# Optimization experiments

Hardware: AMD Instinct MI355X
Metric: run time of the kernel (lower is better)

Reference implementation:

```python
import jax, jax.numpy as jnp
import numpy as np

B, S, D = 2, 2048, 1024
H, DH = 16, 64  # num_heads, attention_dim


def setup_inputs() -> dict:
    key = jax.random.key(0)
    ks = jax.random.split(key, 10)
    x = jax.random.normal(ks[0], (B, S, D), dtype=jnp.float32)
    # causal mask, broadcast over batch and heads (mask==0 -> -inf)
    mask = jnp.tril(jnp.ones((S, S), dtype=jnp.int32))[None, None]
    s = 1.0 / np.sqrt(D)
    Wq = jax.random.normal(ks[1], (D, H * DH), dtype=jnp.float32) * s
    bq = jnp.zeros((H * DH,), dtype=jnp.float32)
    Wk = jax.random.normal(ks[2], (D, H * DH), dtype=jnp.float32) * s
    bk = jnp.zeros((H * DH,), dtype=jnp.float32)
    Wv = jax.random.normal(ks[3], (D, H * DH), dtype=jnp.float32) * s
    bv = jnp.zeros((H * DH,), dtype=jnp.float32)
    Wo = jax.random.normal(ks[4], (H * DH, D), dtype=jnp.float32) * (1.0 / np.sqrt(H * DH))
    bo = jnp.zeros((D,), dtype=jnp.float32)
    return {"x": x, "mask": mask, "Wq": Wq, "bq": bq, "Wk": Wk, "bk": bk,
            "Wv": Wv, "bv": bv, "Wo": Wo, "bo": bo}


def reference(x, mask, Wq, bq, Wk, bk, Wv, bv, Wo, bo):
    b, s, _ = x.shape
    q = (x @ Wq + bq).reshape(b, s, H, DH)
    k = (x @ Wk + bk).reshape(b, s, H, DH)
    v = (x @ Wv + bv).reshape(b, s, H, DH)
    # scores: [B, H, S, S]
    scores = jnp.einsum("bshd,bthd->bhst", q, k) / jnp.sqrt(jnp.float32(DH))
    scores = jnp.where(mask == 0, -jnp.inf, scores)
    w = jax.nn.softmax(scores, axis=-1)
    attended = jnp.einsum("bhst,bthd->bshd", w, v).reshape(b, s, H * DH)
    return attended @ Wo + bo
```

## Files before the change

### kernel.cpp

```cpp
#include <hip/hip_runtime.h>
#include <hip/hip_bf16.h>

#define B_ 2
#define S_ 2048
#define D_ 1024
#define H_ 16
#define DH_ 64

typedef __attribute__((ext_vector_type(8))) short bf16x8;
typedef __attribute__((ext_vector_type(4))) float f32x4;

#define QSCALE 0.18033688011112042f

__device__ __forceinline__ ushort f2b(float f){
  __hip_bfloat16 h = __float2bfloat16(f);
  return *reinterpret_cast<ushort*>(&h);
}

__device__ __forceinline__ unsigned cvtpk(float lo, float hi){
  unsigned r;
  asm("v_cvt_pk_bf16_f32 %0, %1, %2" : "=v"(r) : "v"(lo), "v"(hi));
  return r;
}

__device__ __forceinline__ void gload16(const ushort* g, ushort* l){
  __builtin_amdgcn_global_load_lds((const __attribute__((address_space(1))) unsigned*)g,
                                   (__attribute__((address_space(3))) unsigned*)l, 16, 0, 0);
}

__global__ __launch_bounds__(256) void k_prep(const float* __restrict__ x, ushort* __restrict__ xb,
                                              const float* __restrict__ Wq, const float* __restrict__ Wk,
                                              const float* __restrict__ Wv, const float* __restrict__ Wo,
                                              ushort* __restrict__ WqkvT, ushort* __restrict__ WoT){
  int bid = blockIdx.x, tid = threadIdx.x;
  if (bid < 2048){
    int i = (bid*256 + tid)*8;
    float4 v0 = *(const float4*)(x + i);
    float4 v1 = *(const float4*)(x + i + 4);
    uint4 o;
    o.x = f2b(v0.x) | ((unsigned)f2b(v0.y)<<16);
    o.y = f2b(v0.z) | ((unsigned)f2b(v0.w)<<16);
    o.z = f2b(v1.x) | ((unsigned)f2b(v1.y)<<16);
    o.w = f2b(v1.z) | ((unsigned)f2b(v1.w)<<16);
    *(uint4*)(xb + i) = o;
    return;
  }
  bid -= 2048;
  const int w = bid >> 10, tb = bid & 1023;
  const float* src = (w==0)?Wq:(w==1)?Wk:(w==2)?Wv:Wo;
  ushort* dst = (w==3)?WoT : WqkvT + (size_t)w*(1024*1024);
  __shared__ float tile[32][33];
  const int bx2 = tb & 31, by2 = tb >> 5;
  const int c0 = bx2*32, r0 = by2*32;
  const int tx = tid & 31, ty = tid >> 5;
  #pragma unroll
  for (int i=0;i<4;i++)
    tile[ty + i*8][tx] = src[(size_t)(r0 + ty + i*8)*1024 + c0 + tx];
  __syncthreads();
  #pragma unroll
  for (int i=0;i<4;i++)
    dst[(size_t)(c0 + ty + i*8)*1024 + r0 + tx] = f2b(tile[tx][ty + i*8]);
}

__global__ __launch_bounds__(512, 4) void k_gemm_qkv(const ushort* __restrict__ A,
                                                     const ushort* __restrict__ BT,
                                                     const float* __restrict__ b0p,
                                                     const float* __restrict__ b1p,
                                                     const float* __restrict__ b2p,
                                                     ushort* __restrict__ Cp,
                                                     int M, int N, int K){
  __shared__ ushort As[256*64];
  __shared__ ushort Bs[128*64];
  const int tid = threadIdx.x;
  const int nbn = N >> 7;
  const int bm = blockIdx.x / nbn, bn = blockIdx.x % nbn;
  const int m0 = bm << 8, n0 = bn << 7;
  const int wave = tid >> 6, lane = tid & 63;
  const int wm = (wave >> 1) << 6, wn = (wave & 1) << 6;
  const int lr = lane & 15, lq = lane >> 4;

  f32x4 acc[4][4] = {};

  const int r0 = tid >> 3;
  const int gk = (tid & 7) ^ (r0 & 7);
  const ushort* Agb = A  + (size_t)(m0 + r0)*K + gk*8;
  const ushort* Bgb = BT + (size_t)(n0 + r0)*K + gk*8;
  const int lofs = tid*8;

  for (int kt = 0; kt < K; kt += 64){
    __syncthreads();
    #pragma unroll
    for (int j=0;j<4;j++)
      gload16(Agb + (size_t)j*64*K + kt, &As[lofs + j*4096]);
    #pragma unroll
    for (int j=0;j<2;j++)
      gload16(Bgb + (size_t)j*64*K + kt, &Bs[lofs + j*4096]);
    __syncthreads();
    #pragma unroll
    for (int kk=0;kk<2;kk++){
      bf16x8 af[4], bfr[4];
      #pragma unroll
      for (int i=0;i<4;i++){
        int ra = wm + i*16 + lr;
        af[i]  = *(bf16x8*)&As[ra*64 + (((kk*4+lq) ^ (ra & 7)) << 3)];
        int rb = wn + i*16 + lr;
        bfr[i] = *(bf16x8*)&Bs[rb*64 + (((kk*4+lq) ^ (rb & 7)) << 3)];
      }
      __builtin_amdgcn_s_setprio(1);
      #pragma unroll
      for (int mi=0;mi<4;mi++)
        #pragma unroll
        for (int ni=0;ni<4;ni++)
          acc[mi][ni] = __builtin_amdgcn_mfma_f32_16x16x32_bf16(af[mi], bfr[ni], acc[mi][ni], 0, 0, 0);
      __builtin_amdgcn_s_setprio(0);
    }
  }

  const int seg = n0 >> 10;
  const float* bp = (seg==0 ? b0p : (seg==1 ? b1p : b2p));
  #pragma unroll
  for (int mi=0;mi<4;mi++){
    #pragma unroll
    for (int ni=0;ni<4;ni++){
      int col = n0 + wn + ni*16 + lr;
      int cl = col & 1023;
      float bv = bp[cl];
      int row0 = m0 + wm + mi*16 + lq*4;
      ushort* Qb = Cp;
      if (seg == 0){
        #pragma unroll
        for (int r=0;r<4;r++)
          Qb[(size_t)(row0+r)*1024 + cl] = f2b((acc[mi][ni][r] + bv) * QSCALE);
      } else if (seg == 1){
        ushort* Kb = Qb + (4u<<20);
        #pragma unroll
        for (int r=0;r<4;r++)
          Kb[(size_t)(row0+r)*1024 + cl] = f2b(acc[mi][ni][r] + bv);
      } else {
        ushort* Vt = Qb + (8u<<20);
        int bb = row0 >> 11, srow = row0 & 2047;
        uint2 pk;
        pk.x = cvtpk(acc[mi][ni][0]+bv, acc[mi][ni][1]+bv);
        pk.y = cvtpk(acc[mi][ni][2]+bv, acc[mi][ni][3]+bv);
        *(uint2*)&Vt[((size_t)(bb*1024 + cl))*2048 + srow] = pk;
      }
    }
  }
}

__global__ __launch_bounds__(256) void k_gemm_out(const ushort* __restrict__ A,
                                                  const ushort* __restrict__ BT,
                                                  const float* __restrict__ bias,
                                                  float* __restrict__ Cp,
                                                  int M, int N, int K){
  __shared__ ushort As[128*64];
  __shared__ ushort Bs[128*64];
  const int tid = threadIdx.x;
  const int nbn = N >> 7;
  const int bm = blockIdx.x / nbn, bn = blockIdx.x % nbn;
  const int m0 = bm << 7, n0 = bn << 7;
  const int wave = tid >> 6, lane = tid & 63;
  const int wm = (wave >> 1) << 6, wn = (wave & 1) << 6;
  const int lr = lane & 15, lq = lane >> 4;

  f32x4 acc[4][4] = {};

  const ushort* Ag[4]; const ushort* Bg[4]; int lofs[4];
  #pragma unroll
  for (int j=0;j<4;j++){
    int c = tid + j*256, row = c >> 3, slot = c & 7;
    int gk = slot ^ (row & 7);
    Ag[j] = A  + (size_t)(m0 + row)*K + gk*8;
    Bg[j] = BT + (size_t)(n0 + row)*K + gk*8;
    lofs[j] = c*8;
  }

  for (int kt = 0; kt < K; kt += 64){
    __syncthreads();
    #pragma unroll
    for (int j=0;j<4;j++){
      gload16(Ag[j] + kt, &As[lofs[j]]);
      gload16(Bg[j] + kt, &Bs[lofs[j]]);
    }
    __syncthreads();
    #pragma unroll
    for (int kk=0;kk<2;kk++){
      bf16x8 af[4], bfr[4];
      #pragma unroll
      for (int i=0;i<4;i++){
        int ra = wm + i*16 + lr;
        af[i]  = *(bf16x8*)&As[ra*64 + (((kk*4+lq) ^ (ra & 7)) << 3)];
        int rb = wn + i*16 + lr;
        bfr[i] = *(bf16x8*)&Bs[rb*64 + (((kk*4+lq) ^ (rb & 7)) << 3)];
      }
      __builtin_amdgcn_s_setprio(1);
      #pragma unroll
      for (int mi=0;mi<4;mi++)
        #pragma unroll
        for (int ni=0;ni<4;ni++)
          acc[mi][ni] = __builtin_amdgcn_mfma_f32_16x16x32_bf16(af[mi], bfr[ni], acc[mi][ni], 0, 0, 0);
      __builtin_amdgcn_s_setprio(0);
    }
  }

  #pragma unroll
  for (int mi=0;mi<4;mi++){
    #pragma unroll
    for (int ni=0;ni<4;ni++){
      int col = n0 + wn + ni*16 + lr;
      float bv = bias[col];
      int row0 = m0 + wm + mi*16 + lq*4;
      #pragma unroll
      for (int r=0;r<4;r++)
        Cp[(size_t)(row0+r)*N + col] = acc[mi][ni][r] + bv;
    }
  }
}

__device__ __forceinline__ bf16x8 lds_frag(const ushort* base, int row, int colbytes){
  return *(const bf16x8*)((const char*)base + row*128 + (colbytes ^ ((row & 7) << 4)));
}

__global__ __launch_bounds__(512) void k_attn_mfma(const ushort* __restrict__ Qb,
                                                   const ushort* __restrict__ Kb,
                                                   const ushort* __restrict__ Vtg,
                                                   ushort* __restrict__ Ob,
                                                   float* __restrict__ accP,
                                                   float* __restrict__ mlP){
  __shared__ ushort Ks[2][64*64];
  __shared__ ushort Vs[2][64*64];
  __shared__ ushort Ps[8][16*64];
  const int bid = blockIdx.x;
  int bh, qb, t0, NT, half; bool split;
  if (bid < 512){
    int u = bid >> 5; bh = bid & 31;
    qb = 15 - (u >> 1); half = u & 1; split = true;
    if (half == 0){ t0 = 0;      NT = qb; }
    else          { t0 = qb + 1; NT = 2*qb + 1; }
  } else {
    int s = bid - 512; qb = 7 - (s >> 5); bh = s & 31;
    t0 = 0; NT = 2*qb + 1; half = 0; split = false;
  }
  const bool diag = (!split) || (half == 1);
  const int h = bh & 15, b = bh >> 4;
  const int q0 = qb << 7;
  const int tid = threadIdx.x;
  const int wq = tid >> 6, lane = tid & 63;
  const int ql = lane & 15, g = lane >> 4;
  const int qrow = q0 + wq*16 + ql;

  bf16x8 Qf0, Qf1;
  {
    const ushort* qp = Qb + (size_t)(b*S_ + qrow)*1024 + h*64 + g*8;
    Qf0 = *(const bf16x8*)(qp);
    Qf1 = *(const bf16x8*)(qp + 32);
  }
  bf16x8 ones;
  #pragma unroll
  for (int i=0;i<8;i++) ones[i] = (short)0x3F80;

  float mst = -1e30f;
  f32x4 lsum = {};
  f32x4 acc[4] = {};

  const int r0c = tid >> 3;
  const int gk0 = (tid & 7) ^ (r0c & 7);
  const ushort* Kp0 = Kb  + (size_t)(b*S_ + r0c)*1024 + h*64 + gk0*8;
  const ushort* Vp0 = Vtg + (size_t)(bh*64 + r0c)*2048 + gk0*8;
  const int lo0 = tid*8;

  #define ASTAGE(t, buf) { \
    gload16(Kp0 + (size_t)(t)*65536, &Ks[buf][lo0]); \
    gload16(Vp0 + (t)*64, &Vs[buf][lo0]); }

  char* Pb = (char*)Ps + wq*2048;

  ASTAGE(t0, 0);
  __syncthreads();
  int cur = 0;
  for (int kt = t0; ; ++kt){
    if (kt < NT) ASTAGE(kt+1, cur^1);

    f32x4 sf[4] = {};
    __builtin_amdgcn_s_setprio(1);
    #pragma unroll
    for (int ki=0; ki<4; ++ki){
      bf16x8 kf = lds_frag(Ks[cur], ki*16 + ql, g*16);
      sf[ki] = __builtin_amdgcn_mfma_f32_16x16x32_bf16(kf, Qf0, sf[ki], 0, 0, 0);
    }
    #pragma unroll
    for (int ki=0; ki<4; ++ki){
      bf16x8 kf = lds_frag(Ks[cur], ki*16 + ql, 64 + g*16);
      sf[ki] = __builtin_amdgcn_mfma_f32_16x16x32_bf16(kf, Qf1, sf[ki], 0, 0, 0);
    }
    __builtin_amdgcn_s_setprio(0);

    float s[16];
    #pragma unroll
    for (int ki=0; ki<4; ++ki)
      #pragma unroll
      for (int r=0; r<4; ++r)
        s[ki*4+r] = sf[ki][r];
    if (diag && kt >= NT-1){
      const int th = qrow - kt*64;
      #pragma unroll
      for (int ki=0; ki<4; ++ki)
        #pragma unroll
        for (int r=0; r<4; ++r)
          if (ki*16 + g*4 + r > th) s[ki*4+r] = -1e30f;
    }
    float t0m = fmaxf(fmaxf(s[0], s[1]), s[2]);
    float t1m = fmaxf(fmaxf(s[3], s[4]), s[5]);
    float t2m = fmaxf(fmaxf(s[6], s[7]), s[8]);
    float t3m = fmaxf(fmaxf(s[9], s[10]), s[11]);
    float t4m = fmaxf(fmaxf(s[12], s[13]), s[14]);
    float mt = fmaxf(fmaxf(fmaxf(t0m, t1m), fmaxf(t2m, t3m)), fmaxf(t4m, s[15]));
    mt = fmaxf(mt, __shfl_xor(mt, 16, 64));
    mt = fmaxf(mt, __shfl_xor(mt, 32, 64));
    if (__any(mt > mst + 8.f)){
      float mnew = fmaxf(mst, mt);
      float corr = exp2f(mst - mnew);
      mst = mnew;
      #pragma unroll
      for (int r=0; r<4; ++r){
        float cr = __shfl(corr, g*4 + r, 64);
        lsum[r] *= cr;
        #pragma unroll
        for (int ni=0; ni<4; ++ni) acc[ni][r] *= cr;
      }
    }
    #pragma unroll
    for (int i=0; i<16; ++i) s[i] = exp2f(s[i] - mst);

    #pragma unroll
    for (int ki=0; ki<4; ++ki){
      uint2 uu;
      uu.x = cvtpk(s[ki*4+0], s[ki*4+1]);
      uu.y = cvtpk(s[ki*4+2], s[ki*4+3]);
      *(uint2*)(Pb + ql*128 + ((ki*32 + g*8) ^ ((ql & 7) << 4))) = uu;
    }

    __builtin_amdgcn_s_setprio(1);
    #pragma unroll
    for (int ks=0; ks<2; ++ks){
      bf16x8 pf = *(const bf16x8*)(Pb + ql*128 + ((ks*64 + g*16) ^ ((ql & 7) << 4)));
      #pragma unroll
      for (int ni=0; ni<4; ++ni){
        bf16x8 vf = lds_frag(Vs[cur], ni*16 + ql, ks*64 + g*16);
        acc[ni] = __builtin_amdgcn_mfma_f32_16x16x32_bf16(pf, vf, acc[ni], 0, 0, 0);
      }
      lsum = __builtin_amdgcn_mfma_f32_16x16x32_bf16(pf, ones, lsum, 0, 0, 0);
    }
    __builtin_amdgcn_s_setprio(0);

    if (kt == NT) break;
    __syncthreads();
    cur ^= 1;
  }
  #undef ASTAGE

  if (!split){
    ushort* Op = Ob + (size_t)(b*S_ + q0 + wq*16)*1024 + h*64;
    #pragma unroll
    for (int r=0; r<4; ++r){
      float ir = 1.0f / lsum[r];
      #pragma unroll
      for (int ni=0; ni<4; ++ni)
        Op[(size_t)(g*4 + r)*1024 + ni*16 + ql] = f2b(acc[ni][r] * ir);
    }
  } else {
    const int slot = (qb - 8)*32 + bh;
    const int rbase = half*32768 + slot*128 + wq*16;
    #pragma unroll
    for (int r=0; r<4; ++r){
      const int tr = rbase + g*4 + r;
      float m_row = __shfl(mst, g*4 + r, 64);
      #pragma unroll
      for (int ni=0; ni<4; ++ni)
        accP[(size_t)tr*64 + ni*16 + ql] = acc[ni][r];
      if (ql == 0)
        *(float2*)(mlP + tr*2) = make_float2(m_row, lsum[r]);
    }
  }
}

__global__ __launch_bounds__(512) void k_combine(const float* __restrict__ accP,
                                                 const float* __restrict__ mlP,
                                                 ushort* __restrict__ Ob){
  const int slot = blockIdx.x;
  const int qb = 8 + (slot >> 5), bh = slot & 31;
  const int b = bh >> 4, h = bh & 15;
  const int row = threadIdx.x >> 2, dq = (threadIdx.x & 3) * 16;
  const int trA = slot*128 + row, trB = 32768 + slot*128 + row;
  float2 mlA = *(const float2*)(mlP + trA*2);
  float2 mlB = *(const float2*)(mlP + trB*2);
  float M = fmaxf(mlA.x, mlB.x);
  float wA = exp2f(mlA.x - M), wB = exp2f(mlB.x - M);
  float inv = 1.0f / (mlA.y*wA + mlB.y*wB);
  wA *= inv; wB *= inv;
  const float* pa = accP + (size_t)trA*64 + dq;
  const float* pb = accP + (size_t)trB*64 + dq;
  ushort* op = Ob + (size_t)(b*S_ + qb*128 + row)*1024 + h*64 + dq;
  uint4 o0, o1;
  unsigned ow[8];
  #pragma unroll
  for (int e=0;e<8;e++){
    float2 va = *(const float2*)(pa + e*2);
    float2 vb = *(const float2*)(pb + e*2);
    ow[e] = cvtpk(va.x*wA + vb.x*wB, va.y*wA + vb.y*wB);
  }
  o0.x=ow[0]; o0.y=ow[1]; o0.z=ow[2]; o0.w=ow[3];
  o1.x=ow[4]; o1.y=ow[5]; o1.z=ow[6]; o1.w=ow[7];
  *(uint4*)(op)     = o0;
  *(uint4*)(op + 8) = o1;
}

extern "C" void kernel_launch(void* const* d_in, const int* in_sizes, int n_in,
                              void* d_out, int out_size, void* d_ws, size_t ws_size,
                              hipStream_t stream){
  const float* x  = (const float*)d_in[0];
  const float* Wq = (const float*)d_in[2];
  const float* bq = (const float*)d_in[3];
  const float* Wk = (const float*)d_in[4];
  const float* bk = (const float*)d_in[5];
  const float* Wv = (const float*)d_in[6];
  const float* bv = (const float*)d_in[7];
  const float* Wo = (const float*)d_in[8];
  const float* bo = (const float*)d_in[9];

  char* ws = (char*)d_ws;
  const size_t MB = 1024u*1024u;
  ushort* xb    = (ushort*)(ws + 0);
  ushort* WqkvT = (ushort*)(ws + 8*MB);
  ushort* WoT   = (ushort*)(ws + 14*MB);
  ushort* Qb    = (ushort*)(ws + 16*MB);
  ushort* Kb    = (ushort*)(ws + 24*MB);
  ushort* Vtg   = (ushort*)(ws + 32*MB);
  float*  mlP   = (float*)(ws + 40*MB);
  ushort* attb  = xb;
  float*  accP  = (float*)d_out;

  const int MN = B_*S_;

  k_prep<<<dim3(6144), dim3(256), 0, stream>>>(x, xb, Wq, Wk, Wv, Wo, WqkvT, WoT);

  k_gemm_qkv<<<dim3((MN/256)*(3072/128)), dim3(512), 0, stream>>>(xb, WqkvT, bq, bk, bv, Qb, MN, 3072, 1024);

  k_attn_mfma<<<dim3(768), dim3(512), 0, stream>>>(Qb, Kb, Vtg, attb, accP, mlP);
  k_combine<<<dim3(256), dim3(512), 0, stream>>>(accP, mlP, attb);

  k_gemm_out<<<dim3((MN/128)*(1024/128)), dim3(256), 0, stream>>>(attb, WoT, bo, (float*)d_out, MN, 1024, 1024);
}
```

Baseline: 121.6 us.

## Process two query row-tiles per wave in attention and store bf16 partials

Each wave in the attention kernel now handles 32 query rows as two 16-row tiles. Blocks drop from 512 to 256 threads, so each K fragment loaded from LDS feeds two MFMAs. The running max is now folded into the accumulator init (scores start at -m), and the rescale is applied by a relative delta. The split-KV range is widened to more query blocks, and split partials are normalized and written as bf16 instead of fp32, halving partial traffic for the combine kernel. In exchange, register pressure rises and bf16 partials lose some precision.

```diff
diff --git a/kernel.cpp b/kernel.cpp
--- a/kernel.cpp
+++ b/kernel.cpp
@@ -169,9 +169,9 @@
   #pragma unroll
   for (int j=0;j<4;j++){
     int c = tid + j*256, row = c >> 3, slot = c & 7;
-    int gk = slot ^ (row & 7);
-    Ag[j] = A  + (size_t)(m0 + row)*K + gk*8;
-    Bg[j] = BT + (size_t)(n0 + row)*K + gk*8;
+    int gk2 = slot ^ (row & 7);
+    Ag[j] = A  + (size_t)(m0 + row)*K + gk2*8;
+    Bg[j] = BT + (size_t)(n0 + row)*K + gk2*8;
     lofs[j] = c*8;
   }
 
@@ -221,57 +221,122 @@
   return *(const bf16x8*)((const char*)base + row*128 + (colbytes ^ ((row & 7) << 4)));
 }
 
-__global__ __launch_bounds__(512) void k_attn_mfma(const ushort* __restrict__ Qb,
+__device__ __forceinline__ void softmax_pv(f32x4 (&sf)[4], float& mst, f32x4& lsum, f32x4 (&acc)[4],
+                                           bool diagmask, int th, int g, int ql,
+                                           char* Pb, const ushort* Vcur, bf16x8 ones){
+  if (diagmask){
+    #pragma unroll
+    for (int ki=0;ki<4;++ki)
+      #pragma unroll
+      for (int r=0;r<4;++r)
+        if (ki*16 + g*4 + r > th) sf[ki][r] = -1e30f;
+  }
+  float t0m = fmaxf(fmaxf(sf[0][0], sf[0][1]), sf[0][2]);
+  float t1m = fmaxf(fmaxf(sf[0][3], sf[1][0]), sf[1][1]);
+  float t2m = fmaxf(fmaxf(sf[1][2], sf[1][3]), sf[2][0]);
+  float t3m = fmaxf(fmaxf(sf[2][1], sf[2][2]), sf[2][3]);
+  float t4m = fmaxf(fmaxf(sf[3][0], sf[3][1]), sf[3][2]);
+  float mt = fmaxf(fmaxf(fmaxf(t0m, t1m), fmaxf(t2m, t3m)), fmaxf(t4m, sf[3][3]));
+  mt = fmaxf(mt, __shfl_xor(mt, 16, 64));
+  mt = fmaxf(mt, __shfl_xor(mt, 32, 64));
+  if (__any(mt > 8.f)){
+    float delta = fmaxf(mt, 0.f);
+    mst += delta;
+    float corr = exp2f(-delta);
+    #pragma unroll
+    for (int r=0;r<4;++r){
+      float cr = __shfl(corr, g*4 + r, 64);
+      lsum[r] *= cr;
+      #pragma unroll
+      for (int ni=0;ni<4;++ni) acc[ni][r] *= cr;
+    }
+    #pragma unroll
+    for (int ki=0;ki<4;++ki)
+      #pragma unroll
+      for (int r=0;r<4;++r) sf[ki][r] -= delta;
+  }
+  #pragma unroll
+  for (int ki=0;ki<4;++ki)
+    #pragma unroll
+    for (int r=0;r<4;++r) sf[ki][r] = exp2f(sf[ki][r]);
+  #pragma unroll
+  for (int ki=0;ki<4;++ki){
+    uint2 uu;
+    uu.x = cvtpk(sf[ki][0], sf[ki][1]);
+    uu.y = cvtpk(sf[ki][2], sf[ki][3]);
+    *(uint2*)(Pb + ql*128 + ((ki*32 + g*8) ^ ((ql & 7) << 4))) = uu;
+  }
+  __builtin_amdgcn_s_setprio(1);
+  #pragma unroll
+  for (int ks=0;ks<2;++ks){
+    bf16x8 pf = *(const bf16x8*)(Pb + ql*128 + ((ks*64 + g*16) ^ ((ql & 7) << 4)));
+    #pragma unroll
+    for (int ni=0;ni<4;++ni){
+      bf16x8 vf = lds_frag(Vcur, ni*16 + ql, ks*64 + g*16);
+      acc[ni] = __builtin_amdgcn_mfma_f32_16x16x32_bf16(pf, vf, acc[ni], 0, 0, 0);
+    }
+    lsum = __builtin_amdgcn_mfma_f32_16x16x32_bf16(pf, ones, lsum, 0, 0, 0);
+  }
+  __builtin_amdgcn_s_setprio(0);
+}
+
+__global__ __launch_bounds__(256) void k_attn_mfma(const ushort* __restrict__ Qb,
                                                    const ushort* __restrict__ Kb,
                                                    const ushort* __restrict__ Vtg,
                                                    ushort* __restrict__ Ob,
-                                                   float* __restrict__ accP,
+                                                   ushort* __restrict__ accPb,
                                                    float* __restrict__ mlP){
   __shared__ ushort Ks[2][64*64];
   __shared__ ushort Vs[2][64*64];
-  __shared__ ushort Ps[8][16*64];
+  __shared__ ushort Ps[4][16*64];
   const int bid = blockIdx.x;
-  int bh, qb, t0, NT, half; bool split;
-  if (bid < 512){
-    int u = bid >> 5; bh = bid & 31;
-    qb = 15 - (u >> 1); half = u & 1; split = true;
-    if (half == 0){ t0 = 0;      NT = qb; }
-    else          { t0 = qb + 1; NT = 2*qb + 1; }
+  int bh, qb, t0, NT, hf = 0; bool split;
+  if (bid < 768){
+    int pr = bid >> 5; bh = bid & 31;
+    qb = 15 - (pr >> 1); hf = pr & 1; split = true;
+    if (hf == 0){ t0 = 0;      NT = qb; }
+    else        { t0 = qb + 1; NT = 2*qb + 1; }
   } else {
-    int s = bid - 512; qb = 7 - (s >> 5); bh = s & 31;
-    t0 = 0; NT = 2*qb + 1; half = 0; split = false;
-  }
-  const bool diag = (!split) || (half == 1);
+    int s = bid - 768; qb = 3 - (s >> 5); bh = s & 31;
+    t0 = 0; NT = 2*qb + 1; split = false;
+  }
+  const bool diag = (!split) || (hf == 1);
   const int h = bh & 15, b = bh >> 4;
   const int q0 = qb << 7;
   const int tid = threadIdx.x;
   const int wq = tid >> 6, lane = tid & 63;
   const int ql = lane & 15, g = lane >> 4;
-  const int qrow = q0 + wq*16 + ql;
-
-  bf16x8 Qf0, Qf1;
-  {
-    const ushort* qp = Qb + (size_t)(b*S_ + qrow)*1024 + h*64 + g*8;
-    Qf0 = *(const bf16x8*)(qp);
-    Qf1 = *(const bf16x8*)(qp + 32);
+
+  bf16x8 Qf[2][2];
+  #pragma unroll
+  for (int u=0;u<2;u++){
+    const ushort* qp = Qb + (size_t)(b*S_ + q0 + wq*32 + u*16 + ql)*1024 + h*64 + g*8;
+    Qf[u][0] = *(const bf16x8*)(qp);
+    Qf[u][1] = *(const bf16x8*)(qp + 32);
   }
   bf16x8 ones;
   #pragma unroll
   for (int i=0;i<8;i++) ones[i] = (short)0x3F80;
 
-  float mst = -1e30f;
-  f32x4 lsum = {};
-  f32x4 acc[4] = {};
-
-  const int r0c = tid >> 3;
-  const int gk0 = (tid & 7) ^ (r0c & 7);
+  float mst0 = 0.f, mst1 = 0.f;
+  f32x4 lsum0 = {}, lsum1 = {};
+  f32x4 acc0[4] = {}, acc1[4] = {};
+
+  const int r0c = tid >> 3, cc = tid & 7;
+  const int r1c = r0c + 32;
+  const int gk0 = cc ^ (r0c & 7);
+  const int gk1 = cc ^ (r1c & 7);
   const ushort* Kp0 = Kb  + (size_t)(b*S_ + r0c)*1024 + h*64 + gk0*8;
+  const ushort* Kp1 = Kb  + (size_t)(b*S_ + r1c)*1024 + h*64 + gk1*8;
   const ushort* Vp0 = Vtg + (size_t)(bh*64 + r0c)*2048 + gk0*8;
-  const int lo0 = tid*8;
+  const ushort* Vp1 = Vtg + (size_t)(bh*64 + r1c)*2048 + gk1*8;
+  const int lo0 = tid*8, lo1 = tid*8 + 2048;
 
   #define ASTAGE(t, buf) { \
     gload16(Kp0 + (size_t)(t)*65536, &Ks[buf][lo0]); \
-    gload16(Vp0 + (t)*64, &Vs[buf][lo0]); }
+    gload16(Kp1 + (size_t)(t)*65536, &Ks[buf][lo1]); \
+    gload16(Vp0 + (t)*64, &Vs[buf][lo0]); \
+    gload16(Vp1 + (t)*64, &Vs[buf][lo1]); }
 
   char* Pb = (char*)Ps + wq*2048;
 
@@ -281,77 +346,27 @@
   for (int kt = t0; ; ++kt){
     if (kt < NT) ASTAGE(kt+1, cur^1);
 
-    f32x4 sf[4] = {};
+    f32x4 i0; i0[0]=i0[1]=i0[2]=i0[3] = -mst0;
+    f32x4 i1; i1[0]=i1[1]=i1[2]=i1[3] = -mst1;
+    f32x4 sf0[4] = {i0,i0,i0,i0};
+    f32x4 sf1[4] = {i1,i1,i1,i1};
     __builtin_amdgcn_s_setprio(1);
     #pragma unroll
-    for (int ki=0; ki<4; ++ki){
-      bf16x8 kf = lds_frag(Ks[cur], ki*16 + ql, g*16);
-      sf[ki] = __builtin_amdgcn_mfma_f32_16x16x32_bf16(kf, Qf0, sf[ki], 0, 0, 0);
-    }
-    #pragma unroll
-    for (int ki=0; ki<4; ++ki){
-      bf16x8 kf = lds_frag(Ks[cur], ki*16 + ql, 64 + g*16);
-      sf[ki] = __builtin_amdgcn_mfma_f32_16x16x32_bf16(kf, Qf1, sf[ki], 0, 0, 0);
+    for (int ks=0; ks<2; ++ks){
+      #pragma unroll
+      for (int ki=0; ki<4; ++ki){
+        bf16x8 kf = lds_frag(Ks[cur], ki*16 + ql, ks*64 + g*16);
+        sf0[ki] = __builtin_amdgcn_mfma_f32_16x16x32_bf16(kf, Qf[0][ks], sf0[ki], 0, 0, 0);
+        sf1[ki] = __builtin_amdgcn_mfma_f32_16x16x32_bf16(kf, Qf[1][ks], sf1[ki], 0, 0, 0);
+      }
     }
     __builtin_amdgcn_s_setprio(0);
 
-    float s[16];
-    #pragma unroll
-    for (int ki=0; ki<4; ++ki)
-      #pragma unroll
-      for (int r=0; r<4; ++r)
-        s[ki*4+r] = sf[ki][r];
-    if (diag && kt >= NT-1){
-      const int th = qrow - kt*64;
-      #pragma unroll
-      for (int ki=0; ki<4; ++ki)
-        #pragma unroll
-        for (int r=0; r<4; ++r)
-          if (ki*16 + g*4 + r > th) s[ki*4+r] = -1e30f;
-    }
-    float t0m = fmaxf(fmaxf(s[0], s[1]), s[2]);
-    float t1m = fmaxf(fmaxf(s[3], s[4]), s[5]);
-    float t2m = fmaxf(fmaxf(s[6], s[7]), s[8]);
-    float t3m = fmaxf(fmaxf(s[9], s[10]), s[11]);
-    float t4m = fmaxf(fmaxf(s[12], s[13]), s[14]);
-    float mt = fmaxf(fmaxf(fmaxf(t0m, t1m), fmaxf(t2m, t3m)), fmaxf(t4m, s[15]));
-    mt = fmaxf(mt, __shfl_xor(mt, 16, 64));
-    mt = fmaxf(mt, __shfl_xor(mt, 32, 64));
-    if (__any(mt > mst + 8.f)){
-      float mnew = fmaxf(mst, mt);
-      float corr = exp2f(mst - mnew);
-      mst = mnew;
-      #pragma unroll
-      for (int r=0; r<4; ++r){
-        float cr = __shfl(corr, g*4 + r, 64);
-        lsum[r] *= cr;
-        #pragma unroll
-        for (int ni=0; ni<4; ++ni) acc[ni][r] *= cr;
-      }
-    }
-    #pragma unroll
-    for (int i=0; i<16; ++i) s[i] = exp2f(s[i] - mst);
-
-    #pragma unroll
-    for (int ki=0; ki<4; ++ki){
-      uint2 uu;
-      uu.x = cvtpk(s[ki*4+0], s[ki*4+1]);
-      uu.y = cvtpk(s[ki*4+2], s[ki*4+3]);
-      *(uint2*)(Pb + ql*128 + ((ki*32 + g*8) ^ ((ql & 7) << 4))) = uu;
-    }
-
-    __builtin_amdgcn_s_setprio(1);
-    #pragma unroll
-    for (int ks=0; ks<2; ++ks){
-      bf16x8 pf = *(const bf16x8*)(Pb + ql*128 + ((ks*64 + g*16) ^ ((ql & 7) << 4)));
-      #pragma unroll
-      for (int ni=0; ni<4; ++ni){
-        bf16x8 vf = lds_frag(Vs[cur], ni*16 + ql, ks*64 + g*16);
-        acc[ni] = __builtin_amdgcn_mfma_f32_16x16x32_bf16(pf, vf, acc[ni], 0, 0, 0);
-      }
-      lsum = __builtin_amdgcn_mfma_f32_16x16x32_bf16(pf, ones, lsum, 0, 0, 0);
-    }
-    __builtin_amdgcn_s_setprio(0);
+    const bool dm = diag && (kt >= 2*qb);
+    softmax_pv(sf0, mst0, lsum0, acc0, dm, q0 + wq*32 + ql - kt*64,      g, ql, Pb, Ks[0] == Ks[0] ? Vs[cur] : Vs[cur], ones);
+    asm volatile("s_waitcnt lgkmcnt(0)" ::: "memory");
+    __builtin_amdgcn_sched_barrier(0);
+    softmax_pv(sf1, mst1, lsum1, acc1, dm, q0 + wq*32 + 16 + ql - kt*64, g, ql, Pb, Vs[cur], ones);
 
     if (kt == NT) break;
     __syncthreads();
@@ -360,55 +375,72 @@
   #undef ASTAGE
 
   if (!split){
-    ushort* Op = Ob + (size_t)(b*S_ + q0 + wq*16)*1024 + h*64;
-    #pragma unroll
-    for (int r=0; r<4; ++r){
-      float ir = 1.0f / lsum[r];
-      #pragma unroll
-      for (int ni=0; ni<4; ++ni)
-        Op[(size_t)(g*4 + r)*1024 + ni*16 + ql] = f2b(acc[ni][r] * ir);
+    #pragma unroll
+    for (int u=0; u<2; ++u){
+      ushort* Op = Ob + (size_t)(b*S_ + q0 + wq*32 + u*16)*1024 + h*64;
+      const f32x4* ac = u ? acc1 : acc0;
+      const f32x4& ls = u ? lsum1 : lsum0;
+      #pragma unroll
+      for (int r=0; r<4; ++r){
+        float ir = 1.0f / ls[r];
+        #pragma unroll
+        for (int ni=0; ni<4; ++ni)
+          Op[(size_t)(g*4 + r)*1024 + ni*16 + ql] = f2b(ac[ni][r] * ir);
+      }
     }
   } else {
-    const int slot = (qb - 8)*32 + bh;
-    const int rbase = half*32768 + slot*128 + wq*16;
-    #pragma unroll
-    for (int r=0; r<4; ++r){
-      const int tr = rbase + g*4 + r;
-      float m_row = __shfl(mst, g*4 + r, 64);
-      #pragma unroll
-      for (int ni=0; ni<4; ++ni)
-        accP[(size_t)tr*64 + ni*16 + ql] = acc[ni][r];
-      if (ql == 0)
-        *(float2*)(mlP + tr*2) = make_float2(m_row, lsum[r]);
-    }
-  }
-}
-
-__global__ __launch_bounds__(512) void k_combine(const float* __restrict__ accP,
+    const int slot = (qb - 4)*32 + bh;
+    #pragma unroll
+    for (int u=0; u<2; ++u){
+      const f32x4* ac = u ? acc1 : acc0;
+      const f32x4& ls = u ? lsum1 : lsum0;
+      float ms = u ? mst1 : mst0;
+      const int rbase = hf*49152 + slot*128 + wq*32 + u*16;
+      #pragma unroll
+      for (int r=0; r<4; ++r){
+        const int tr = rbase + g*4 + r;
+        float ir = 1.0f / ls[r];
+        float m_row = __shfl(ms, g*4 + r, 64);
+        #pragma unroll
+        for (int ni=0; ni<4; ++ni)
+          accPb[(size_t)tr*64 + ni*16 + ql] = f2b(ac[ni][r] * ir);
+        if (ql == 0)
+          *(float2*)(mlP + tr*2) = make_float2(m_row, ls[r]);
+      }
+    }
+  }
+}
+
+__global__ __launch_bounds__(512) void k_combine(const ushort* __restrict__ accPb,
                                                  const float* __restrict__ mlP,
                                                  ushort* __restrict__ Ob){
   const int slot = blockIdx.x;
-  const int qb = 8 + (slot >> 5), bh = slot & 31;
+  const int qb = 4 + (slot >> 5), bh = slot & 31;
   const int b = bh >> 4, h = bh & 15;
   const int row = threadIdx.x >> 2, dq = (threadIdx.x & 3) * 16;
-  const int trA = slot*128 + row, trB = 32768 + slot*128 + row;
+  const int trA = slot*128 + row, trB = 49152 + slot*128 + row;
   float2 mlA = *(const float2*)(mlP + trA*2);
   float2 mlB = *(const float2*)(mlP + trB*2);
   float M = fmaxf(mlA.x, mlB.x);
-  float wA = exp2f(mlA.x - M), wB = exp2f(mlB.x - M);
-  float inv = 1.0f / (mlA.y*wA + mlB.y*wB);
+  float wA = mlA.y * exp2f(mlA.x - M);
+  float wB = mlB.y * exp2f(mlB.x - M);
+  float inv = 1.0f / (wA + wB);
   wA *= inv; wB *= inv;
-  const float* pa = accP + (size_t)trA*64 + dq;
-  const float* pb = accP + (size_t)trB*64 + dq;
+  const ushort* pa = accPb + (size_t)trA*64 + dq;
+  const ushort* pb = accPb + (size_t)trB*64 + dq;
+  uint4 a0 = *(const uint4*)pa, a1 = *(const uint4*)(pa + 8);
+  uint4 b0 = *(const uint4*)pb, b1 = *(const uint4*)(pb + 8);
+  unsigned aw[8] = {a0.x,a0.y,a0.z,a0.w,a1.x,a1.y,a1.z,a1.w};
+  unsigned bw[8] = {b0.x,b0.y,b0.z,b0.w,b1.x,b1.y,b1.z,b1.w};
+  unsigned ow[8];
+  #pragma unroll
+  for (int e=0;e<8;e++){
+    float alo = __uint_as_float(aw[e] << 16), ahi = __uint_as_float(aw[e] & 0xffff0000u);
+    float blo = __uint_as_float(bw[e] << 16), bhi = __uint_as_float(bw[e] & 0xffff0000u);
+    ow[e] = cvtpk(alo*wA + blo*wB, ahi*wA + bhi*wB);
+  }
   ushort* op = Ob + (size_t)(b*S_ + qb*128 + row)*1024 + h*64 + dq;
   uint4 o0, o1;
-  unsigned ow[8];
-  #pragma unroll
-  for (int e=0;e<8;e++){
-    float2 va = *(const float2*)(pa + e*2);
-    float2 vb = *(const float2*)(pb + e*2);
-    ow[e] = cvtpk(va.x*wA + vb.x*wB, va.y*wA + vb.y*wB);
-  }
   o0.x=ow[0]; o0.y=ow[1]; o0.z=ow[2]; o0.w=ow[3];
   o1.x=ow[4]; o1.y=ow[5]; o1.z=ow[6]; o1.w=ow[7];
   *(uint4*)(op)     = o0;
@@ -438,7 +470,7 @@
   ushort* Vtg   = (ushort*)(ws + 32*MB);
   float*  mlP   = (float*)(ws + 40*MB);
   ushort* attb  = xb;
-  float*  accP  = (float*)d_out;
+  ushort* accPb = (ushort*)d_out;
 
   const int MN = B_*S_;
 
@@ -446,8 +478,8 @@
 
   k_gemm_qkv<<<dim3((MN/256)*(3072/128)), dim3(512), 0, stream>>>(xb, WqkvT, bq, bk, bv, Qb, MN, 3072, 1024);
 
-  k_attn_mfma<<<dim3(768), dim3(512), 0, stream>>>(Qb, Kb, Vtg, attb, accP, mlP);
-  k_combine<<<dim3(256), dim3(512), 0, stream>>>(accP, mlP, attb);
+  k_attn_mfma<<<dim3(896), dim3(256), 0, stream>>>(Qb, Kb, Vtg, attb, accPb, mlP);
+  k_combine<<<dim3(384), dim3(512), 0, stream>>>(accPb, mlP, attb);
 
   k_gemm_out<<<dim3((MN/128)*(1024/128)), dim3(256), 0, stream>>>(attb, WoT, bo, (float*)d_out, MN, 1024, 1024);
 }
```

Result: slower. 125.7 us (+3.4%).
